# Optimization experiments

Measured on AMD Instinct MI355X. Metric: run time of the kernel, lower is better.

## Reference

```python
import jax, jax.numpy as jnp
import numpy as np

B, NP, C_IN, H = 8, 6250, 512, 256   # graphs, nodes/graph, in-feat, hidden
EPG = 100000                          # edges per graph
K = 5000                              # ceil(0.8 * NP) kept by TopKPooling
H3 = 3 * H


def setup_inputs() -> dict:
    key = jax.random.key(0)
    ks = jax.random.split(key, 16)
    N, E = B * NP, B * EPG
    x = jax.random.normal(ks[0], (N, C_IN), jnp.float32)
    offs = (jnp.arange(E) // EPG) * NP  # keep edges inside their graph
    src = jax.random.randint(ks[1], (E,), 0, NP) + offs
    dst = jax.random.randint(ks[2], (E,), 0, NP) + offs
    edge_index = jnp.stack([src, dst]).astype(jnp.int64)
    edge_attr = jax.random.uniform(ks[3], (E,), jnp.float32)
    batch = jnp.repeat(jnp.arange(B), NP).astype(jnp.int64)
    s = 0.05
    W1 = jax.random.normal(ks[4], (C_IN, H), jnp.float32) * s
    b1 = jnp.zeros((H,), jnp.float32)
    W2 = jax.random.normal(ks[5], (H, H), jnp.float32) * s
    b2 = jnp.zeros((H,), jnp.float32)
    pw = jax.random.normal(ks[6], (H3,), jnp.float32) * s   # TopKPooling attn vector
    lw1 = jax.random.normal(ks[7], (H3 * 2, H), jnp.float32) * s
    lb1 = jnp.zeros((H,), jnp.float32)
    lw2 = jax.random.normal(ks[8], (H, H // 2), jnp.float32) * s
    lb2 = jnp.zeros((H // 2,), jnp.float32)
    lw3 = jax.random.normal(ks[9], (H // 2, 3), jnp.float32) * s
    lb3 = jnp.zeros((3,), jnp.float32)
    return {"x": x, "edge_index": edge_index, "edge_attr": edge_attr, "batch": batch,
            "W1": W1, "b1": b1, "W2": W2, "b2": b2, "pw": pw,
            "lw1": lw1, "lb1": lb1, "lw2": lw2, "lb2": lb2, "lw3": lw3, "lb3": lb3}


def _gcn(x, W, b, src, dst, ew, n):
    xw = x @ W
    deg = jnp.zeros((n,), xw.dtype).at[dst].add(ew) + 1.0
    dinv = jax.lax.rsqrt(deg)
    norm = dinv[src] * ew * dinv[dst]
    out = jnp.zeros_like(xw).at[dst].add(norm[:, None] * xw[src])
    return out + (dinv * dinv)[:, None] * xw + b


def reference(x, edge_index, edge_attr, batch, W1, b1, W2, b2, pw,
              lw1, lb1, lw2, lb2, lw3, lb3):
    N = x.shape[0]
    src, dst = edge_index[0], edge_index[1]
    x1 = jax.nn.relu(_gcn(x, W1, b1, src, dst, edge_attr, N))
    x2 = jax.nn.relu(_gcn(x1, W2, b2, src, dst, edge_attr, N))
    x3 = jax.nn.relu(_gcn(x2, W2, b2, src, dst, edge_attr, N))  # conv2 reused (as in source)
    cat_x = jnp.concatenate([x1, x2, x3], axis=1)               # [N, 3H]
    # TopKPooling: score = sigmoid((x . w) / ||w||), keep top-K per graph, scale by score
    score = jax.nn.sigmoid((cat_x @ pw) / jnp.linalg.norm(pw))   # [N]
    sc = score.reshape(B, NP)
    topv, topi = jax.lax.top_k(sc, K)                            # [B, K]
    xg = cat_x.reshape(B, NP, H3)
    sel = jnp.take_along_axis(xg, topi[:, :, None], axis=1) * topv[:, :, None]  # [B, K, 3H]
    readout = jnp.concatenate([sel.mean(axis=1), sel.max(axis=1)], axis=1)      # [B, 6H]
    h = jax.nn.relu(readout @ lw1 + lb1)
    h = jax.nn.relu(h @ lw2 + lb2)       # dropout p=0 is a no-op
    return h @ lw3 + lb3                 # [B, 3]
```

## Files before the change

### kernel.cpp

```cpp
#include <hip/hip_runtime.h>
#include <stdint.h>

#define NODES  50000
#define MPAD   50048
#define NGRAPH 8
#define NP_G   6250
#define EPG    100000
#define EDGES  800000
#define KKEEP  5000
#define HID    256
#define CIN    512
#define H3     768
#define SCANB  196
#define RCHUNK 200
#define MLPCH  24
#define MLPCK  64
#define ESL    3125

#define K1_HIST  512
#define K1_CAST  25000
#define K1_W1    512
#define K1_W2    256
#define K1_TOTAL (K1_HIST + K1_CAST + K1_W1 + K1_W2 + 1)
#define GEMM_GRID 784
#define K2_GEMM  GEMM_GRID
#define K2_FILL  256
#define K2_TOTAL (K2_GEMM + K2_FILL)

using f32x4  = __attribute__((ext_vector_type(4))) float;
using bf16x8 = __attribute__((ext_vector_type(8))) short;
using u16x8  = __attribute__((ext_vector_type(8))) unsigned short;
typedef unsigned short u16;
typedef unsigned int   u32;
typedef unsigned long long u64;

__device__ __forceinline__ float bf2f(u16 u) {
    return __uint_as_float(((uint32_t)u) << 16);
}
__device__ __forceinline__ u16 f2bf(float f) {
    uint32_t u = __float_as_uint(f);
    u += 0x7fffu + ((u >> 16) & 1u);
    return (u16)(u >> 16);
}

__global__ __launch_bounds__(256) void k1_kernel(
        const int* __restrict__ ei, const float* __restrict__ ew,
        u64* __restrict__ partial,
        const float* __restrict__ x, u16* __restrict__ A0,
        const float* __restrict__ W1, const float* __restrict__ W2,
        const float* __restrict__ pw,
        u16* __restrict__ Wt1, u16* __restrict__ Wt2, float* __restrict__ invn) {
    __shared__ __align__(16) char smem[ESL * 8];
    int b = blockIdx.x, t = threadIdx.x;
    if (b < K1_HIST) {
        u64* hl = (u64*)smem;
        int g  = b >> 6;
        int r  = b & 63;
        int bb = r >> 1;
        int h  = r & 1;
        for (int k = t; k < ESL; k += 256) hl[k] = 0ull;
        __syncthreads();
        int ebase = g * EPG + bb * ESL;
        int lo = h * ESL;
        for (int k = t; k < ESL; k += 256) {
            int e = ebase + k;
            int d = ei[EDGES + e];
            int il = d - g * NP_G - lo;
            if ((unsigned)il < (unsigned)ESL) {
                u64 enc = (1ull << 48) | (u64)(ew[e] * 4294967296.0f);
                atomicAdd(&hl[il], enc);
            }
        }
        __syncthreads();
        u64* prow = partial + (size_t)(g * 32 + bb) * NP_G + lo;
        for (int k = t; k < ESL; k += 256) prow[k] = hl[k];
    } else if (b < K1_HIST + K1_CAST) {
        size_t base = ((size_t)(b - K1_HIST) * 256 + t) * 4;
        float4 v = *(const float4*)(x + base);
        ushort4 o;
        o.x = f2bf(v.x); o.y = f2bf(v.y); o.z = f2bf(v.z); o.w = f2bf(v.w);
        *(ushort4*)(A0 + base) = o;
    } else if (b < K1_HIST + K1_CAST + K1_W1) {
        int id = (b - K1_HIST - K1_CAST) * 256 + t;
        int n = id >> 9, k = id & 511;
        Wt1[id] = f2bf(W1[(size_t)k * HID + n]);
    } else if (b < K1_TOTAL - 1) {
        int id = (b - K1_HIST - K1_CAST - K1_W1) * 256 + t;
        int n = id >> 8, k = id & 255;
        Wt2[id] = f2bf(W2[(size_t)k * HID + n]);
    } else {
        float* sh = (float*)smem;
        float s = 0.f;
        for (int i = t; i < H3; i += 256) { float v = pw[i]; s += v * v; }
        sh[t] = s; __syncthreads();
        for (int off = 128; off; off >>= 1) {
            if (t < off) sh[t] += sh[t + off];
            __syncthreads();
        }
        if (t == 0) invn[0] = rsqrtf(sh[0]);
    }
}

__global__ void scan1_kernel(const u64* __restrict__ partial,
                             u32* __restrict__ blockbase,
                             int* __restrict__ iscan, int* __restrict__ bsum,
                             float* __restrict__ dinv) {
    int b = blockIdx.x, t = threadIdx.x;
    int i = b * 256 + t;
    int c = 0;
    if (i < NODES) {
        int g = i / NP_G, il = i - g * NP_G;
        size_t base = (size_t)(g * 32) * NP_G + il;
        u64 fix = 0ull; u32 cnt = 0;
#pragma unroll 4
        for (int j = 0; j < 32; ++j) {
            size_t idx = base + (size_t)j * NP_G;
            u64 pv = partial[idx];
            blockbase[idx] = cnt;
            cnt += (u32)(pv >> 48);
            fix += pv & 0xFFFFFFFFFFFFull;
        }
        c = (int)cnt;
        float deg = (float)fix * (1.0f / 4294967296.0f);
        dinv[i] = rsqrtf(deg + 1.0f);
    }
    int lane = t & 63, wv = t >> 6;
    int v = c;
    for (int off = 1; off < 64; off <<= 1) {
        int u = __shfl_up(v, off);
        if (lane >= off) v += u;
    }
    __shared__ int ws[4];
    if (lane == 63) ws[wv] = v;
    __syncthreads();
    if (t == 0) { int s = 0; for (int k = 0; k < 4; k++) { int tmp = ws[k]; ws[k] = s; s += tmp; } }
    __syncthreads();
    v += ws[wv];
    if (i < NODES) iscan[i] = v - c;
    if (t == 255) bsum[b] = v;
}

__global__ void scan2_kernel(const int* __restrict__ bsum, int* __restrict__ boff) {
    int t = threadIdx.x;
    int c = (t < SCANB) ? bsum[t] : 0;
    int lane = t & 63, wv = t >> 6;
    int v = c;
    for (int off = 1; off < 64; off <<= 1) {
        int u = __shfl_up(v, off);
        if (lane >= off) v += u;
    }
    __shared__ int ws[4];
    if (lane == 63) ws[wv] = v;
    __syncthreads();
    if (t == 0) { int s = 0; for (int k = 0; k < 4; k++) { int tmp = ws[k]; ws[k] = s; s += tmp; } }
    __syncthreads();
    v += ws[wv];
    if (t < SCANB) boff[t] = v - c;
}

__global__ void scan3_kernel(const int* __restrict__ iscan, const int* __restrict__ boff,
                             int* __restrict__ rowptr) {
    int b = blockIdx.x, t = threadIdx.x;
    int i = b * 256 + t;
    if (i > NODES) return;
    if (i == NODES) { rowptr[NODES] = EDGES; return; }
    rowptr[i] = boff[b] + iscan[i];
}

__device__ __forceinline__ bool gemm_map(int i, int& bm, int& bn) {
    int g = i & 7, s = i >> 3;
    int cnt = (g == 5) ? 48 : 49;
    if ((s >> 1) >= cnt) return false;
    bm = 49 * g - (g > 5 ? 1 : 0) + (s >> 1);
    bn = s & 1;
    return true;
}

__device__ __forceinline__ void gemm_body(const u16* __restrict__ A,
                                          const u16* __restrict__ Bt,
                                          u16* __restrict__ C,
                                          int K, int bm, int bn,
                                          u16* As, u16* Bs) {
    const int tid  = threadIdx.x;
    const int wave = tid >> 6, lane = tid & 63;
    const int wm = wave >> 1, wn = wave & 1;
    const int quad = lane >> 4, l16 = lane & 15;
    const int sr = tid >> 2;
    const int sc = tid & 3;
    const int swz = (sc ^ ((sr >> 1) & 3)) * 8;
    const int rphys = (quad ^ ((l16 >> 1) & 3)) * 8;

    const u16* Ag = A + (size_t)(bm * 128 + sr) * K + sc * 8;
    const u16* Bg = Bt + (size_t)(bn * 128 + sr) * K + sc * 8;

    f32x4 acc[4][4];
#pragma unroll
    for (int i = 0; i < 4; i++)
#pragma unroll
        for (int j = 0; j < 4; j++) { f32x4 z = {0.f, 0.f, 0.f, 0.f}; acc[i][j] = z; }

    for (int k0 = 0; k0 < K; k0 += 32) {
        int4 av0 = *(const int4*)(Ag + k0);
        int4 av1 = *(const int4*)(Ag + (size_t)64 * K + k0);
        int4 bv0 = *(const int4*)(Bg + k0);
        int4 bv1 = *(const int4*)(Bg + (size_t)64 * K + k0);
        __syncthreads();
        *(int4*)(As + sr * 32 + swz)        = av0;
        *(int4*)(As + (sr + 64) * 32 + swz) = av1;
        *(int4*)(Bs + sr * 32 + swz)        = bv0;
        *(int4*)(Bs + (sr + 64) * 32 + swz) = bv1;
        __syncthreads();
        bf16x8 af[4], bfr[4];
#pragma unroll
        for (int i = 0; i < 4; i++)
            af[i] = *(const bf16x8*)(As + (wm * 64 + i * 16 + l16) * 32 + rphys);
#pragma unroll
        for (int j = 0; j < 4; j++)
            bfr[j] = *(const bf16x8*)(Bs + (wn * 64 + j * 16 + l16) * 32 + rphys);
#pragma unroll
        for (int i = 0; i < 4; i++)
#pragma unroll
            for (int j = 0; j < 4; j++)
                acc[i][j] = __builtin_amdgcn_mfma_f32_16x16x32_bf16(af[i], bfr[j], acc[i][j], 0, 0, 0);
    }

    const int crow0 = bm * 128 + wm * 64 + quad * 4;
    const int ccol0 = bn * 128 + wn * 64 + l16;
#pragma unroll
    for (int i = 0; i < 4; i++)
#pragma unroll
        for (int j = 0; j < 4; j++)
#pragma unroll
            for (int r = 0; r < 4; r++)
                C[(size_t)(crow0 + i * 16 + r) * HID + ccol0 + j * 16] = f2bf(acc[i][j][r]);
}

__global__ __launch_bounds__(256) void k2_kernel(
        const u16* __restrict__ A0, const u16* __restrict__ Wt1, u16* __restrict__ xw,
        const int* __restrict__ ei, const float* __restrict__ ew,
        const float* __restrict__ dinv, const int* __restrict__ rowptr,
        const u32* __restrict__ blockbase, int2* __restrict__ csr) {
    __shared__ __align__(16) char smem[NP_G * 4];
    int b = blockIdx.x;
    if (b < K2_GEMM) {
        int bm, bn;
        if (!gemm_map(b, bm, bn)) return;
        u16* As = (u16*)smem;
        u16* Bs = (u16*)(smem + 8192);
        gemm_body(A0, Wt1, xw, CIN, bm, bn, As, Bs);
    } else {
        u32* cursor = (u32*)smem;
        int g  = b & 7;
        int bb = (b - K2_GEMM) >> 3;
        const u32* bbase = blockbase + (size_t)(g * 32 + bb) * NP_G;
        const int* rp = rowptr + g * NP_G;
        for (int k = threadIdx.x; k < NP_G; k += 256)
            cursor[k] = (u32)rp[k] + bbase[k];
        __syncthreads();
        int ebase = g * EPG + bb * ESL;
#pragma unroll 4
        for (int k = threadIdx.x; k < ESL; k += 256) {
            int e = ebase + k;
            int s = ei[e], d = ei[EDGES + e];
            int il = d - g * NP_G;
            u32 pos = atomicAdd(&cursor[il], 1u);
            csr[pos] = make_int2(s, __float_as_int(dinv[s] * ew[e] * dinv[d]));
        }
    }
}

__global__ __launch_bounds__(256) void gemm_bt(const u16* __restrict__ A,
                                               const u16* __restrict__ Bt,
                                               u16* __restrict__ C, int K) {
    __shared__ u16 As[128 * 32];
    __shared__ u16 Bs[128 * 32];
    int bm, bn;
    if (!gemm_map(blockIdx.x, bm, bn)) return;
    gemm_body(A, Bt, C, K, bm, bn, As, Bs);
}

template<bool SCORE>
__global__ void agg_kernel(const u16* __restrict__ xw, u16* __restrict__ xo,
                           const int* __restrict__ rowptr, const int2* __restrict__ csr,
                           const float* __restrict__ dinv, const float* __restrict__ bias,
                           const u16* __restrict__ xs1, const u16* __restrict__ xs2,
                           const float* __restrict__ pw, const float* __restrict__ invn,
                           float* __restrict__ score, u64* __restrict__ keys) {
    int wave = threadIdx.x >> 6;
    int lane = threadIdx.x & 63;
    int g  = blockIdx.x & 7;
    int nl = (blockIdx.x >> 3) * 4 + wave;
    if (nl >= NP_G) return;
    int w = g * NP_G + nl;
    int half = lane >> 5;
    int f8 = (lane & 31) * 8;
    size_t ro = (size_t)w * HID + f8;

    float acc0[8], acc1[8];
#pragma unroll
    for (int j = 0; j < 8; ++j) { acc0[j] = 0.f; acc1[j] = 0.f; }

    int p = rowptr[w], p1 = rowptr[w + 1];
    for (int q = p; q < p1; q += 64) {
        int m = min(64, p1 - q);
        int2 e = make_int2(0, 0);
        if (lane < m) e = csr[q + lane];
        int j = 0;
        for (; j + 8 <= m; j += 8) {
            int i0 = j + half,     i1 = j + 2 + half;
            int i2 = j + 4 + half, i3 = j + 6 + half;
            int   s0 = __shfl(e.x, i0, 64); float w0 = __int_as_float(__shfl(e.y, i0, 64));
            int   s1 = __shfl(e.x, i1, 64); float w1 = __int_as_float(__shfl(e.y, i1, 64));
            int   s2 = __shfl(e.x, i2, 64); float w2 = __int_as_float(__shfl(e.y, i2, 64));
            int   s3 = __shfl(e.x, i3, 64); float w3 = __int_as_float(__shfl(e.y, i3, 64));
            u16x8 v0 = *(const u16x8*)(xw + (size_t)s0 * HID + f8);
            u16x8 v1 = *(const u16x8*)(xw + (size_t)s1 * HID + f8);
            u16x8 v2 = *(const u16x8*)(xw + (size_t)s2 * HID + f8);
            u16x8 v3 = *(const u16x8*)(xw + (size_t)s3 * HID + f8);
#pragma unroll
            for (int t = 0; t < 8; ++t) {
                acc0[t] += w0 * bf2f(v0[t]);
                acc1[t] += w1 * bf2f(v1[t]);
                acc0[t] += w2 * bf2f(v2[t]);
                acc1[t] += w3 * bf2f(v3[t]);
            }
        }
        for (; j + 2 <= m; j += 2) {
            int i0 = j + half;
            int s0 = __shfl(e.x, i0, 64); float w0 = __int_as_float(__shfl(e.y, i0, 64));
            u16x8 v0 = *(const u16x8*)(xw + (size_t)s0 * HID + f8);
#pragma unroll
            for (int t = 0; t < 8; ++t) acc0[t] += w0 * bf2f(v0[t]);
        }
        if (j < m) {
            int s0 = __shfl(e.x, j, 64); float w0 = __int_as_float(__shfl(e.y, j, 64));
            w0 = half ? 0.f : w0;
            u16x8 v0 = *(const u16x8*)(xw + (size_t)s0 * HID + f8);
#pragma unroll
            for (int t = 0; t < 8; ++t) acc0[t] += w0 * bf2f(v0[t]);
        }
    }

#pragma unroll
    for (int j = 0; j < 8; ++j) {
        acc0[j] += acc1[j];
        acc0[j] += __shfl(acc0[j], lane ^ 32, 64);
    }

    float di = dinv[w], sw = di * di;
    u16x8 sv = *(const u16x8*)(xw + ro);
    float bb[8];
    {
        float4 t0 = *(const float4*)(bias + f8);
        float4 t1 = *(const float4*)(bias + f8 + 4);
        bb[0] = t0.x; bb[1] = t0.y; bb[2] = t0.z; bb[3] = t0.w;
        bb[4] = t1.x; bb[5] = t1.y; bb[6] = t1.z; bb[7] = t1.w;
    }
    u16x8 o;
    float ov[8];
#pragma unroll
    for (int j = 0; j < 8; ++j) {
        float v = fmaxf(acc0[j] + sw * bf2f(sv[j]) + bb[j], 0.f);
        o[j] = f2bf(v);
        ov[j] = bf2f(o[j]);
    }
    if (half == 0) *(u16x8*)(xo + ro) = o;

    if (SCORE) {
        u16x8 v1 = *(const u16x8*)(xs1 + ro);
        u16x8 v2 = *(const u16x8*)(xs2 + ro);
        float acc = 0.f;
#pragma unroll
        for (int j = 0; j < 8; ++j) {
            acc += bf2f(v1[j]) * pw[f8 + j];
            acc += bf2f(v2[j]) * pw[256 + f8 + j];
            acc += ov[j]       * pw[512 + f8 + j];
        }
#pragma unroll
        for (int off = 1; off < 32; off <<= 1) acc += __shfl_xor(acc, off, 64);
        if (lane == 0) {
            float s = acc * invn[0];
            float sc = 1.f / (1.f + __expf(-s));
            score[w] = sc;
            keys[w] = ((u64)__float_as_uint(sc) << 13) | (unsigned int)(NP_G - 1 - nl);
        }
    }
}

__global__ __launch_bounds__(1024) void selcomp_kernel(
        const u64* __restrict__ keys, const float* __restrict__ score,
        int* __restrict__ selidx, float* __restrict__ selscr) {
    __shared__ u64 kk[NP_G];
    __shared__ unsigned int hist[4][256];
    __shared__ unsigned int sfx[257];
    __shared__ u64 spref;
    __shared__ unsigned int swant;
    int g = blockIdx.x, t = threadIdx.x;
    const u64* kg = keys + (size_t)g * NP_G;
    for (int i = t; i < NP_G; i += 1024) kk[i] = kg[i];
    if (t == 0) { spref = 0ull; swant = KKEEP; }
    const int wgrp = (t >> 8) & 3;
    u64 mask = 0ull;
    __syncthreads();
    for (int shift = 40; shift >= 0; shift -= 8) {
        if (t < 256) { hist[0][t] = 0; hist[1][t] = 0; hist[2][t] = 0; hist[3][t] = 0; }
        __syncthreads();
        u64 pref = spref;
        for (int i = t; i < NP_G; i += 1024) {
            u64 key = kk[i];
            if ((key & mask) == pref)
                atomicAdd(&hist[wgrp][(unsigned int)(key >> shift) & 255u], 1u);
        }
        __syncthreads();
        if (t < 256) sfx[t] = hist[0][t] + hist[1][t] + hist[2][t] + hist[3][t];
        if (t == 0) sfx[256] = 0;
        __syncthreads();
        for (int off = 1; off < 256; off <<= 1) {
            unsigned int v = 0;
            if (t < 256 && t + off < 256) v = sfx[t + off];
            __syncthreads();
            if (t < 256 && t + off < 256) sfx[t] += v;
            __syncthreads();
        }
        unsigned int want = swant;
        __syncthreads();
        if (t < 256) {
            unsigned int s0 = sfx[t], s1 = sfx[t + 1];
            if (s0 >= want && s1 < want) {
                spref = pref | ((u64)t << shift);
                swant = want - s1;
            }
        }
        __syncthreads();
        mask |= (255ull << shift);
    }
    u64 kth = spref;
    int lane = t & 63, wv = t >> 6;
    __shared__ int wsum[16];
    __shared__ int cbase;
    if (t == 0) cbase = 0;
    __syncthreads();
    for (int k = 0; k < (NP_G + 1023) / 1024; ++k) {
        int i = k * 1024 + t;
        bool sel = (i < NP_G) && (kk[i] >= kth);
        int n = g * NP_G + i;
        u64 bal = __ballot(sel);
        int prefix = __popcll(bal & ((1ull << lane) - 1ull));
        if (lane == 0) wsum[wv] = __popcll(bal);
        __syncthreads();
        if (t == 0) {
            int s = cbase;
            for (int j = 0; j < 16; ++j) { int tmp = wsum[j]; wsum[j] = s; s += tmp; }
            cbase = s;
        }
        __syncthreads();
        if (sel) {
            int pos = wsum[wv] + prefix;
            selidx[g * KKEEP + pos] = n;
            selscr[g * KKEEP + pos] = score[n];
        }
        __syncthreads();
    }
}

__global__ __launch_bounds__(256) void readout_kernel(
        const u16* __restrict__ x1, const u16* __restrict__ x2,
        const u16* __restrict__ x3,
        const int* __restrict__ selidx, const float* __restrict__ selscr,
        float* __restrict__ sumbuf, int* __restrict__ maxbuf) {
    int g = blockIdx.x, tpart = blockIdx.y, c = blockIdx.z;
    int fcol = threadIdx.x;
    const u16* xt = (tpart == 0) ? x1 : ((tpart == 1) ? x2 : x3);
    __shared__ int   sidx[RCHUNK];
    __shared__ float sscr[RCHUNK];
    int base = g * KKEEP + c * RCHUNK;
    if (fcol < RCHUNK) { sidx[fcol] = selidx[base + fcol]; sscr[fcol] = selscr[base + fcol]; }
    __syncthreads();
    float sum = 0.f, mx = 0.f;
#pragma unroll 1
    for (int j = 0; j < RCHUNK; j += 4) {
        int n0 = sidx[j], n1 = sidx[j + 1], n2 = sidx[j + 2], n3 = sidx[j + 3];
        float s0 = sscr[j], s1 = sscr[j + 1], s2 = sscr[j + 2], s3 = sscr[j + 3];
        float v0 = bf2f(xt[(size_t)n0 * HID + fcol]) * s0;
        float v1 = bf2f(xt[(size_t)n1 * HID + fcol]) * s1;
        float v2 = bf2f(xt[(size_t)n2 * HID + fcol]) * s2;
        float v3 = bf2f(xt[(size_t)n3 * HID + fcol]) * s3;
        sum += v0 + v1 + v2 + v3;
        mx = fmaxf(mx, fmaxf(fmaxf(v0, v1), fmaxf(v2, v3)));
    }
    int o = (g * 3 + tpart) * HID + fcol;
    atomicAdd(&sumbuf[o], sum);
    atomicMax(&maxbuf[o], __float_as_int(mx));
}

__global__ __launch_bounds__(256) void mlp1_kernel(const float* __restrict__ sumbuf,
                                                   const int* __restrict__ maxbuf,
                                                   const float* __restrict__ lw1,
                                                   float* __restrict__ h1acc) {
    int g = blockIdx.x, ch = blockIdx.y, t = threadIdx.x;
    __shared__ float r[MLPCK];
    int k0 = ch * MLPCK;
    if (t < MLPCK) {
        int i = k0 + t;
        r[t] = (i < 768) ? sumbuf[g * 768 + i] * (1.f / 5000.f)
                         : __int_as_float(maxbuf[g * 768 + (i - 768)]);
    }
    __syncthreads();
    float a0 = 0.f, a1 = 0.f, a2 = 0.f, a3 = 0.f;
#pragma unroll
    for (int i = 0; i < MLPCK; i += 4) {
        a0 += r[i]     * lw1[(size_t)(k0 + i)     * 256 + t];
        a1 += r[i + 1] * lw1[(size_t)(k0 + i + 1) * 256 + t];
        a2 += r[i + 2] * lw1[(size_t)(k0 + i + 2) * 256 + t];
        a3 += r[i + 3] * lw1[(size_t)(k0 + i + 3) * 256 + t];
    }
    atomicAdd(&h1acc[g * 256 + t], (a0 + a1) + (a2 + a3));
}

__global__ __launch_bounds__(256) void mlp2_kernel(const float* __restrict__ h1acc,
                                                   const float* __restrict__ lb1,
                                                   const float* __restrict__ lw2,
                                                   const float* __restrict__ lb2,
                                                   const float* __restrict__ lw3,
                                                   const float* __restrict__ lb3,
                                                   float* __restrict__ out) {
    __shared__ float h1[256];
    __shared__ float part[256];
    __shared__ float h2[128];
    int g = blockIdx.x, t = threadIdx.x;
    h1[t] = fmaxf(h1acc[g * 256 + t] + lb1[t], 0.f);
    __syncthreads();
    int col = t & 127, half = t >> 7;
    float a = 0.f;
#pragma unroll
    for (int i = 0; i < 128; i += 4) {
        int k = half * 128 + i;
        a += h1[k]     * lw2[k * 128 + col]
           + h1[k + 1] * lw2[(k + 1) * 128 + col]
           + h1[k + 2] * lw2[(k + 2) * 128 + col]
           + h1[k + 3] * lw2[(k + 3) * 128 + col];
    }
    part[t] = a;
    __syncthreads();
    if (t < 128) h2[t] = fmaxf(part[t] + part[t + 128] + lb2[t], 0.f);
    __syncthreads();
    if (t < 3) {
        float a3 = lb3[t];
        for (int i = 0; i < 128; ++i) a3 += h2[i] * lw3[i * 3 + t];
        out[g * 3 + t] = a3;
    }
}

extern "C" void kernel_launch(void* const* d_in, const int* in_sizes, int n_in,
                              void* d_out, int out_size, void* d_ws, size_t ws_size,
                              hipStream_t stream) {
    const float* x   = (const float*)d_in[0];
    const int*   ei  = (const int*)d_in[1];
    const float* ew  = (const float*)d_in[2];
    const float* W1  = (const float*)d_in[4];
    const float* b1  = (const float*)d_in[5];
    const float* W2  = (const float*)d_in[6];
    const float* b2  = (const float*)d_in[7];
    const float* pw  = (const float*)d_in[8];
    const float* lw1 = (const float*)d_in[9];
    const float* lb1 = (const float*)d_in[10];
    const float* lw2 = (const float*)d_in[11];
    const float* lb2 = (const float*)d_in[12];
    const float* lw3 = (const float*)d_in[13];
    const float* lb3 = (const float*)d_in[14];
    float* out = (float*)d_out;

    char* p = (char*)d_ws;
    auto alloc = [&](size_t bytes) -> char* {
        char* r = p;
        p += (bytes + 255) & ~(size_t)255;
        return r;
    };
    u16* A0  = (u16*)alloc((size_t)MPAD * CIN * 2);
    u16* x3  = (u16*)alloc((size_t)MPAD * HID * 2);
    u16* xw  = (u16*)alloc((size_t)MPAD * HID * 2);
    u16* Wt1 = (u16*)alloc((size_t)HID * CIN * 2);
    u16* Wt2 = (u16*)alloc((size_t)HID * HID * 2);
    int2*  csr    = (int2*)alloc((size_t)EDGES * 8);
    u64*   partial   = (u64*)alloc((size_t)256 * NP_G * 8);
    u32*   blockbase = (u32*)alloc((size_t)256 * NP_G * 4);
    int*   rowptr = (int*)alloc((size_t)(NODES + 1) * 4);
    int*   iscan  = (int*)alloc((size_t)NODES * 4);
    int*   bsum   = (int*)alloc((size_t)SCANB * 4);
    int*   boff   = (int*)alloc((size_t)SCANB * 4);
    u64*   keys   = (u64*)alloc((size_t)NODES * 8);
    float* score  = (float*)alloc((size_t)NODES * 4);
    float* dinv   = (float*)alloc((size_t)NODES * 4);
    int*   selidx = (int*)alloc((size_t)NGRAPH * KKEEP * 4);
    float* selscr = (float*)alloc((size_t)NGRAPH * KKEEP * 4);
    float* invn   = (float*)alloc(256);
    char* zbase = p;
    float* sumbuf = (float*)alloc(6144 * 4);
    int*   maxbuf = (int*)alloc(6144 * 4);
    float* h1acc  = (float*)alloc((size_t)NGRAPH * 256 * 4);
    size_t zbytes = (size_t)(p - zbase);

    u16* x1 = A0;
    u16* x2 = A0 + (size_t)MPAD * HID;

    hipMemsetAsync(zbase, 0, zbytes, stream);

    k1_kernel<<<K1_TOTAL, 256, 0, stream>>>(ei, ew, partial, x, A0,
                                            W1, W2, pw, Wt1, Wt2, invn);
    scan1_kernel<<<SCANB, 256, 0, stream>>>(partial, blockbase, iscan, bsum, dinv);
    scan2_kernel<<<1, 256, 0, stream>>>(bsum, boff);
    scan3_kernel<<<SCANB + 1, 256, 0, stream>>>(iscan, boff, rowptr);
    k2_kernel<<<K2_TOTAL, 256, 0, stream>>>(A0, Wt1, xw, ei, ew, dinv, rowptr,
                                            blockbase, csr);

    int aggBlocks = 8 * ((NP_G + 3) / 4);

    agg_kernel<false><<<aggBlocks, 256, 0, stream>>>(xw, x1, rowptr, csr, dinv, b1,
                                                     nullptr, nullptr, nullptr, nullptr,
                                                     nullptr, nullptr);
    gemm_bt<<<GEMM_GRID, 256, 0, stream>>>(x1, Wt2, xw, HID);
    agg_kernel<false><<<aggBlocks, 256, 0, stream>>>(xw, x2, rowptr, csr, dinv, b2,
                                                     nullptr, nullptr, nullptr, nullptr,
                                                     nullptr, nullptr);
    gemm_bt<<<GEMM_GRID, 256, 0, stream>>>(x2, Wt2, xw, HID);
    agg_kernel<true><<<aggBlocks, 256, 0, stream>>>(xw, x3, rowptr, csr, dinv, b2,
                                                    x1, x2, pw, invn, score, keys);

    selcomp_kernel<<<NGRAPH, 1024, 0, stream>>>(keys, score, selidx, selscr);
    readout_kernel<<<dim3(NGRAPH, 3, KKEEP / RCHUNK), 256, 0, stream>>>(
        x1, x2, x3, selidx, selscr, sumbuf, maxbuf);
    mlp1_kernel<<<dim3(NGRAPH, MLPCH), 256, 0, stream>>>(sumbuf, maxbuf, lw1, h1acc);
    mlp2_kernel<<<NGRAPH, 256, 0, stream>>>(h1acc, lb1, lw2, lb2, lw3, lb3, out);
}
```

Measured before the change: 462.8 us.

## Fuse fp32-to-bf16 cast into first GEMM, merge scan passes, unroll aggregation

Drops the separate pass that cast the node-feature matrix to bf16 and wrote it out. The first GEMM now loads fp32 rows and converts them in registers with packed bf16 conversion instructions, which removes one full write and re-read of a large intermediate. The scan2 kernel is folded into scan3: each block sums the preceding block totals itself, saving one launch at the cost of redundant reductions. The aggregation loop gains a 16-edge unrolled path to put more gathers in flight, which raises register pressure. The GEMM now also reads twice as many A bytes per tile.

```diff
diff --git a/kernel.cpp b/kernel.cpp
--- a/kernel.cpp
+++ b/kernel.cpp
@@ -18,10 +18,9 @@
 #define ESL    3125
 
 #define K1_HIST  512
-#define K1_CAST  25000
 #define K1_W1    512
 #define K1_W2    256
-#define K1_TOTAL (K1_HIST + K1_CAST + K1_W1 + K1_W2 + 1)
+#define K1_TOTAL (K1_HIST + K1_W1 + K1_W2 + 1)
 #define GEMM_GRID 784
 #define K2_GEMM  GEMM_GRID
 #define K2_FILL  256
@@ -42,11 +41,18 @@
     u += 0x7fffu + ((u >> 16) & 1u);
     return (u16)(u >> 16);
 }
+__device__ __forceinline__ int4 f32x8_to_bf16x8(float4 a, float4 b) {
+    int4 r;
+    asm("v_cvt_pk_bf16_f32 %0, %1, %2" : "=v"(r.x) : "v"(a.x), "v"(a.y));
+    asm("v_cvt_pk_bf16_f32 %0, %1, %2" : "=v"(r.y) : "v"(a.z), "v"(a.w));
+    asm("v_cvt_pk_bf16_f32 %0, %1, %2" : "=v"(r.z) : "v"(b.x), "v"(b.y));
+    asm("v_cvt_pk_bf16_f32 %0, %1, %2" : "=v"(r.w) : "v"(b.z), "v"(b.w));
+    return r;
+}
 
 __global__ __launch_bounds__(256) void k1_kernel(
         const int* __restrict__ ei, const float* __restrict__ ew,
         u64* __restrict__ partial,
-        const float* __restrict__ x, u16* __restrict__ A0,
         const float* __restrict__ W1, const float* __restrict__ W2,
         const float* __restrict__ pw,
         u16* __restrict__ Wt1, u16* __restrict__ Wt2, float* __restrict__ invn) {
@@ -74,18 +80,12 @@
         __syncthreads();
         u64* prow = partial + (size_t)(g * 32 + bb) * NP_G + lo;
         for (int k = t; k < ESL; k += 256) prow[k] = hl[k];
-    } else if (b < K1_HIST + K1_CAST) {
-        size_t base = ((size_t)(b - K1_HIST) * 256 + t) * 4;
-        float4 v = *(const float4*)(x + base);
-        ushort4 o;
-        o.x = f2bf(v.x); o.y = f2bf(v.y); o.z = f2bf(v.z); o.w = f2bf(v.w);
-        *(ushort4*)(A0 + base) = o;
-    } else if (b < K1_HIST + K1_CAST + K1_W1) {
-        int id = (b - K1_HIST - K1_CAST) * 256 + t;
+    } else if (b < K1_HIST + K1_W1) {
+        int id = (b - K1_HIST) * 256 + t;
         int n = id >> 9, k = id & 511;
         Wt1[id] = f2bf(W1[(size_t)k * HID + n]);
     } else if (b < K1_TOTAL - 1) {
-        int id = (b - K1_HIST - K1_CAST - K1_W1) * 256 + t;
+        int id = (b - K1_HIST - K1_W1) * 256 + t;
         int n = id >> 8, k = id & 255;
         Wt2[id] = f2bf(W2[(size_t)k * HID + n]);
     } else {
@@ -140,31 +140,19 @@
     if (t == 255) bsum[b] = v;
 }
 
-__global__ void scan2_kernel(const int* __restrict__ bsum, int* __restrict__ boff) {
-    int t = threadIdx.x;
-    int c = (t < SCANB) ? bsum[t] : 0;
-    int lane = t & 63, wv = t >> 6;
-    int v = c;
-    for (int off = 1; off < 64; off <<= 1) {
-        int u = __shfl_up(v, off);
-        if (lane >= off) v += u;
-    }
-    __shared__ int ws[4];
-    if (lane == 63) ws[wv] = v;
-    __syncthreads();
-    if (t == 0) { int s = 0; for (int k = 0; k < 4; k++) { int tmp = ws[k]; ws[k] = s; s += tmp; } }
-    __syncthreads();
-    v += ws[wv];
-    if (t < SCANB) boff[t] = v - c;
-}
-
-__global__ void scan3_kernel(const int* __restrict__ iscan, const int* __restrict__ boff,
+__global__ void scan3_kernel(const int* __restrict__ iscan, const int* __restrict__ bsum,
                              int* __restrict__ rowptr) {
     int b = blockIdx.x, t = threadIdx.x;
+    int v = (t < b) ? bsum[t] : 0;
+    for (int off = 1; off < 64; off <<= 1) v += __shfl_xor(v, off, 64);
+    __shared__ int ws[4];
+    if ((t & 63) == 0) ws[t >> 6] = v;
+    __syncthreads();
+    int boffb = ws[0] + ws[1] + ws[2] + ws[3];
     int i = b * 256 + t;
     if (i > NODES) return;
     if (i == NODES) { rowptr[NODES] = EDGES; return; }
-    rowptr[i] = boff[b] + iscan[i];
+    rowptr[i] = boffb + iscan[i];
 }
 
 __device__ __forceinline__ bool gemm_map(int i, int& bm, int& bn) {
@@ -235,8 +223,74 @@
                 C[(size_t)(crow0 + i * 16 + r) * HID + ccol0 + j * 16] = f2bf(acc[i][j][r]);
 }
 
+__device__ __forceinline__ void gemm_body_f32A(const float* __restrict__ X,
+                                               const u16* __restrict__ Bt,
+                                               u16* __restrict__ C,
+                                               int bm, int bn,
+                                               u16* As, u16* Bs) {
+    const int tid  = threadIdx.x;
+    const int wave = tid >> 6, lane = tid & 63;
+    const int wm = wave >> 1, wn = wave & 1;
+    const int quad = lane >> 4, l16 = lane & 15;
+    const int sr = tid >> 2;
+    const int sc = tid & 3;
+    const int swz = (sc ^ ((sr >> 1) & 3)) * 8;
+    const int rphys = (quad ^ ((l16 >> 1) & 3)) * 8;
+
+    int r0 = bm * 128 + sr;      if (r0 > NODES - 1) r0 = NODES - 1;
+    int r1 = bm * 128 + sr + 64; if (r1 > NODES - 1) r1 = NODES - 1;
+    const float* Ag0 = X + (size_t)r0 * CIN + sc * 8;
+    const float* Ag1 = X + (size_t)r1 * CIN + sc * 8;
+    const u16*   Bg  = Bt + (size_t)(bn * 128 + sr) * CIN + sc * 8;
+
+    f32x4 acc[4][4];
+#pragma unroll
+    for (int i = 0; i < 4; i++)
+#pragma unroll
+        for (int j = 0; j < 4; j++) { f32x4 z = {0.f, 0.f, 0.f, 0.f}; acc[i][j] = z; }
+
+    for (int k0 = 0; k0 < CIN; k0 += 32) {
+        float4 a00 = *(const float4*)(Ag0 + k0);
+        float4 a01 = *(const float4*)(Ag0 + k0 + 4);
+        float4 a10 = *(const float4*)(Ag1 + k0);
+        float4 a11 = *(const float4*)(Ag1 + k0 + 4);
+        int4 bv0 = *(const int4*)(Bg + k0);
+        int4 bv1 = *(const int4*)(Bg + (size_t)64 * CIN + k0);
+        int4 av0 = f32x8_to_bf16x8(a00, a01);
+        int4 av1 = f32x8_to_bf16x8(a10, a11);
+        __syncthreads();
+        *(int4*)(As + sr * 32 + swz)        = av0;
+        *(int4*)(As + (sr + 64) * 32 + swz) = av1;
+        *(int4*)(Bs + sr * 32 + swz)        = bv0;
+        *(int4*)(Bs + (sr + 64) * 32 + swz) = bv1;
+        __syncthreads();
+        bf16x8 af[4], bfr[4];
+#pragma unroll
+        for (int i = 0; i < 4; i++)
+            af[i] = *(const bf16x8*)(As + (wm * 64 + i * 16 + l16) * 32 + rphys);
+#pragma unroll
+        for (int j = 0; j < 4; j++)
+            bfr[j] = *(const bf16x8*)(Bs + (wn * 64 + j * 16 + l16) * 32 + rphys);
+#pragma unroll
+        for (int i = 0; i < 4; i++)
+#pragma unroll
+            for (int j = 0; j < 4; j++)
+                acc[i][j] = __builtin_amdgcn_mfma_f32_16x16x32_bf16(af[i], bfr[j], acc[i][j], 0, 0, 0);
+    }
+
+    const int crow0 = bm * 128 + wm * 64 + quad * 4;
+    const int ccol0 = bn * 128 + wn * 64 + l16;
+#pragma unroll
+    for (int i = 0; i < 4; i++)
+#pragma unroll
+        for (int j = 0; j < 4; j++)
+#pragma unroll
+            for (int r = 0; r < 4; r++)
+                C[(size_t)(crow0 + i * 16 + r) * HID + ccol0 + j * 16] = f2bf(acc[i][j][r]);
+}
+
 __global__ __launch_bounds__(256) void k2_kernel(
-        const u16* __restrict__ A0, const u16* __restrict__ Wt1, u16* __restrict__ xw,
+        const float* __restrict__ x, const u16* __restrict__ Wt1, u16* __restrict__ xw,
         const int* __restrict__ ei, const float* __restrict__ ew,
         const float* __restrict__ dinv, const int* __restrict__ rowptr,
         const u32* __restrict__ blockbase, int2* __restrict__ csr) {
@@ -247,7 +301,7 @@
         if (!gemm_map(b, bm, bn)) return;
         u16* As = (u16*)smem;
         u16* Bs = (u16*)(smem + 8192);
-        gemm_body(A0, Wt1, xw, CIN, bm, bn, As, Bs);
+        gemm_body_f32A(x, Wt1, xw, bm, bn, As, Bs);
     } else {
         u32* cursor = (u32*)smem;
         int g  = b & 7;
@@ -306,6 +360,27 @@
         int2 e = make_int2(0, 0);
         if (lane < m) e = csr[q + lane];
         int j = 0;
+        for (; j + 16 <= m; j += 16) {
+            int   s[8]; float wt[8];
+#pragma unroll
+            for (int k = 0; k < 8; ++k) {
+                int idx = j + 2 * k + half;
+                s[k]  = __shfl(e.x, idx, 64);
+                wt[k] = __int_as_float(__shfl(e.y, idx, 64));
+            }
+            u16x8 v[8];
+#pragma unroll
+            for (int k = 0; k < 8; ++k)
+                v[k] = *(const u16x8*)(xw + (size_t)s[k] * HID + f8);
+#pragma unroll
+            for (int k = 0; k < 8; k += 2) {
+#pragma unroll
+                for (int t = 0; t < 8; ++t) {
+                    acc0[t] += wt[k]     * bf2f(v[k][t]);
+                    acc1[t] += wt[k + 1] * bf2f(v[k + 1][t]);
+                }
+            }
+        }
         for (; j + 8 <= m; j += 8) {
             int i0 = j + half,     i1 = j + 2 + half;
             int i2 = j + 4 + half, i3 = j + 6 + half;
@@ -587,7 +662,6 @@
     int*   rowptr = (int*)alloc((size_t)(NODES + 1) * 4);
     int*   iscan  = (int*)alloc((size_t)NODES * 4);
     int*   bsum   = (int*)alloc((size_t)SCANB * 4);
-    int*   boff   = (int*)alloc((size_t)SCANB * 4);
     u64*   keys   = (u64*)alloc((size_t)NODES * 8);
     float* score  = (float*)alloc((size_t)NODES * 4);
     float* dinv   = (float*)alloc((size_t)NODES * 4);
@@ -605,12 +679,11 @@
 
     hipMemsetAsync(zbase, 0, zbytes, stream);
 
-    k1_kernel<<<K1_TOTAL, 256, 0, stream>>>(ei, ew, partial, x, A0,
+    k1_kernel<<<K1_TOTAL, 256, 0, stream>>>(ei, ew, partial,
                                             W1, W2, pw, Wt1, Wt2, invn);
     scan1_kernel<<<SCANB, 256, 0, stream>>>(partial, blockbase, iscan, bsum, dinv);
-    scan2_kernel<<<1, 256, 0, stream>>>(bsum, boff);
-    scan3_kernel<<<SCANB + 1, 256, 0, stream>>>(iscan, boff, rowptr);
-    k2_kernel<<<K2_TOTAL, 256, 0, stream>>>(A0, Wt1, xw, ei, ew, dinv, rowptr,
+    scan3_kernel<<<SCANB + 1, 256, 0, stream>>>(iscan, bsum, rowptr);
+    k2_kernel<<<K2_TOTAL, 256, 0, stream>>>(x, Wt1, xw, ei, ew, dinv, rowptr,
                                             blockbase, csr);
 
     int aggBlocks = 8 * ((NP_G + 3) / 4);
```

Result: slower. 472.7 us (+2.1%).

## Split GEMM and CSR fill kernels, shrink GEMM tile, fold scan2 into scan3

Applied to the files above, without the earlier changes.

Shrinks the bf16 MFMA GEMM tile from 128x128 to 64x128 rows per block, doubling the grid and cutting LDS and accumulator registers so more blocks fit per CU. The first GEMM no longer shares a launch with the CSR fill. The fill becomes its own kernel that uses a half-size shared cursor array and makes two passes over each edge slice. The separate scan2 launch is dropped: each scan3 block reduces the preceding block sums itself. This saves a launch at the cost of redundant reductions, and the fill now reads the destination indices twice.

```diff
diff --git a/kernel.cpp b/kernel.cpp
--- a/kernel.cpp
+++ b/kernel.cpp
@@ -22,10 +22,8 @@
 #define K1_W1    512
 #define K1_W2    256
 #define K1_TOTAL (K1_HIST + K1_CAST + K1_W1 + K1_W2 + 1)
-#define GEMM_GRID 784
-#define K2_GEMM  GEMM_GRID
-#define K2_FILL  256
-#define K2_TOTAL (K2_GEMM + K2_FILL)
+#define GEMM_GRID 1568
+#define FILL_GRID 256
 
 using f32x4  = __attribute__((ext_vector_type(4))) float;
 using bf16x8 = __attribute__((ext_vector_type(8))) short;
@@ -140,143 +138,136 @@
     if (t == 255) bsum[b] = v;
 }
 
-__global__ void scan2_kernel(const int* __restrict__ bsum, int* __restrict__ boff) {
-    int t = threadIdx.x;
-    int c = (t < SCANB) ? bsum[t] : 0;
-    int lane = t & 63, wv = t >> 6;
-    int v = c;
-    for (int off = 1; off < 64; off <<= 1) {
-        int u = __shfl_up(v, off);
-        if (lane >= off) v += u;
-    }
-    __shared__ int ws[4];
-    if (lane == 63) ws[wv] = v;
-    __syncthreads();
-    if (t == 0) { int s = 0; for (int k = 0; k < 4; k++) { int tmp = ws[k]; ws[k] = s; s += tmp; } }
-    __syncthreads();
-    v += ws[wv];
-    if (t < SCANB) boff[t] = v - c;
-}
-
-__global__ void scan3_kernel(const int* __restrict__ iscan, const int* __restrict__ boff,
+__global__ void scan3_kernel(const int* __restrict__ iscan, const int* __restrict__ bsum,
                              int* __restrict__ rowptr) {
     int b = blockIdx.x, t = threadIdx.x;
+    int v = (t < b) ? bsum[t] : 0;
+    for (int off = 1; off < 64; off <<= 1) v += __shfl_xor(v, off, 64);
+    __shared__ int ws[4];
+    if ((t & 63) == 0) ws[t >> 6] = v;
+    __syncthreads();
+    int boffb = ws[0] + ws[1] + ws[2] + ws[3];
     int i = b * 256 + t;
     if (i > NODES) return;
     if (i == NODES) { rowptr[NODES] = EDGES; return; }
-    rowptr[i] = boff[b] + iscan[i];
-}
-
-__device__ __forceinline__ bool gemm_map(int i, int& bm, int& bn) {
+    rowptr[i] = boffb + iscan[i];
+}
+
+__device__ __forceinline__ bool gemm_map64(int i, int& bm, int& bn) {
     int g = i & 7, s = i >> 3;
-    int cnt = (g == 5) ? 48 : 49;
-    if ((s >> 1) >= cnt) return false;
-    bm = 49 * g - (g > 5 ? 1 : 0) + (s >> 1);
+    int b0 = (6250 * g + 63) >> 6;
+    int b1 = (6250 * (g + 1) + 63) >> 6;
+    int t = b0 + (s >> 1);
+    if (t >= b1) return false;
+    bm = t;
     bn = s & 1;
     return true;
 }
 
-__device__ __forceinline__ void gemm_body(const u16* __restrict__ A,
-                                          const u16* __restrict__ Bt,
-                                          u16* __restrict__ C,
-                                          int K, int bm, int bn,
-                                          u16* As, u16* Bs) {
+__device__ __forceinline__ void gemm64_body(const u16* __restrict__ A,
+                                            const u16* __restrict__ Bt,
+                                            u16* __restrict__ C,
+                                            int K, int bm, int bn,
+                                            u16* As, u16* Bs) {
     const int tid  = threadIdx.x;
     const int wave = tid >> 6, lane = tid & 63;
-    const int wm = wave >> 1, wn = wave & 1;
     const int quad = lane >> 4, l16 = lane & 15;
     const int sr = tid >> 2;
     const int sc = tid & 3;
     const int swz = (sc ^ ((sr >> 1) & 3)) * 8;
     const int rphys = (quad ^ ((l16 >> 1) & 3)) * 8;
 
-    const u16* Ag = A + (size_t)(bm * 128 + sr) * K + sc * 8;
+    const u16* Ag = A + (size_t)(bm * 64 + sr) * K + sc * 8;
     const u16* Bg = Bt + (size_t)(bn * 128 + sr) * K + sc * 8;
 
-    f32x4 acc[4][4];
+    f32x4 acc[4][2];
 #pragma unroll
     for (int i = 0; i < 4; i++)
 #pragma unroll
-        for (int j = 0; j < 4; j++) { f32x4 z = {0.f, 0.f, 0.f, 0.f}; acc[i][j] = z; }
+        for (int j = 0; j < 2; j++) { f32x4 z = {0.f, 0.f, 0.f, 0.f}; acc[i][j] = z; }
 
     for (int k0 = 0; k0 < K; k0 += 32) {
         int4 av0 = *(const int4*)(Ag + k0);
-        int4 av1 = *(const int4*)(Ag + (size_t)64 * K + k0);
         int4 bv0 = *(const int4*)(Bg + k0);
         int4 bv1 = *(const int4*)(Bg + (size_t)64 * K + k0);
         __syncthreads();
         *(int4*)(As + sr * 32 + swz)        = av0;
-        *(int4*)(As + (sr + 64) * 32 + swz) = av1;
         *(int4*)(Bs + sr * 32 + swz)        = bv0;
         *(int4*)(Bs + (sr + 64) * 32 + swz) = bv1;
         __syncthreads();
-        bf16x8 af[4], bfr[4];
+        bf16x8 af[4], bfr[2];
 #pragma unroll
         for (int i = 0; i < 4; i++)
-            af[i] = *(const bf16x8*)(As + (wm * 64 + i * 16 + l16) * 32 + rphys);
-#pragma unroll
-        for (int j = 0; j < 4; j++)
-            bfr[j] = *(const bf16x8*)(Bs + (wn * 64 + j * 16 + l16) * 32 + rphys);
+            af[i] = *(const bf16x8*)(As + (i * 16 + l16) * 32 + rphys);
+#pragma unroll
+        for (int j = 0; j < 2; j++)
+            bfr[j] = *(const bf16x8*)(Bs + (wave * 32 + j * 16 + l16) * 32 + rphys);
 #pragma unroll
         for (int i = 0; i < 4; i++)
 #pragma unroll
-            for (int j = 0; j < 4; j++)
+            for (int j = 0; j < 2; j++)
                 acc[i][j] = __builtin_amdgcn_mfma_f32_16x16x32_bf16(af[i], bfr[j], acc[i][j], 0, 0, 0);
     }
 
-    const int crow0 = bm * 128 + wm * 64 + quad * 4;
-    const int ccol0 = bn * 128 + wn * 64 + l16;
+    const int crow0 = bm * 64 + quad * 4;
+    const int ccol0 = bn * 128 + wave * 32 + l16;
 #pragma unroll
     for (int i = 0; i < 4; i++)
 #pragma unroll
-        for (int j = 0; j < 4; j++)
+        for (int j = 0; j < 2; j++)
 #pragma unroll
             for (int r = 0; r < 4; r++)
                 C[(size_t)(crow0 + i * 16 + r) * HID + ccol0 + j * 16] = f2bf(acc[i][j][r]);
 }
 
 __global__ __launch_bounds__(256) void k2_kernel(
-        const u16* __restrict__ A0, const u16* __restrict__ Wt1, u16* __restrict__ xw,
+        const u16* __restrict__ A0, const u16* __restrict__ Wt1,
+        u16* __restrict__ C) {
+    __shared__ u16 As[64 * 32];
+    __shared__ u16 Bs[128 * 32];
+    int bm, bn;
+    if (!gemm_map64(blockIdx.x, bm, bn)) return;
+    gemm64_body(A0, Wt1, C, CIN, bm, bn, As, Bs);
+}
+
+__global__ __launch_bounds__(256) void gemm_bt(const u16* __restrict__ A,
+                                               const u16* __restrict__ Bt,
+                                               u16* __restrict__ C, int K) {
+    __shared__ u16 As[64 * 32];
+    __shared__ u16 Bs[128 * 32];
+    int bm, bn;
+    if (!gemm_map64(blockIdx.x, bm, bn)) return;
+    gemm64_body(A, Bt, C, K, bm, bn, As, Bs);
+}
+
+__global__ __launch_bounds__(256) void fill_kernel(
         const int* __restrict__ ei, const float* __restrict__ ew,
         const float* __restrict__ dinv, const int* __restrict__ rowptr,
         const u32* __restrict__ blockbase, int2* __restrict__ csr) {
-    __shared__ __align__(16) char smem[NP_G * 4];
-    int b = blockIdx.x;
-    if (b < K2_GEMM) {
-        int bm, bn;
-        if (!gemm_map(b, bm, bn)) return;
-        u16* As = (u16*)smem;
-        u16* Bs = (u16*)(smem + 8192);
-        gemm_body(A0, Wt1, xw, CIN, bm, bn, As, Bs);
-    } else {
-        u32* cursor = (u32*)smem;
-        int g  = b & 7;
-        int bb = (b - K2_GEMM) >> 3;
-        const u32* bbase = blockbase + (size_t)(g * 32 + bb) * NP_G;
-        const int* rp = rowptr + g * NP_G;
-        for (int k = threadIdx.x; k < NP_G; k += 256)
-            cursor[k] = (u32)rp[k] + bbase[k];
-        __syncthreads();
-        int ebase = g * EPG + bb * ESL;
+    __shared__ u32 cursor[ESL];
+    int g  = blockIdx.x & 7;
+    int bb = blockIdx.x >> 3;
+    const u32* bbase = blockbase + (size_t)(g * 32 + bb) * NP_G;
+    const int* rp = rowptr + g * NP_G;
+    int ebase = g * EPG + bb * ESL;
+    for (int h = 0; h < 2; ++h) {
+        int lo = h * ESL;
+        for (int k = threadIdx.x; k < ESL; k += 256)
+            cursor[k] = (u32)rp[lo + k] + bbase[lo + k];
+        __syncthreads();
 #pragma unroll 4
         for (int k = threadIdx.x; k < ESL; k += 256) {
             int e = ebase + k;
-            int s = ei[e], d = ei[EDGES + e];
-            int il = d - g * NP_G;
-            u32 pos = atomicAdd(&cursor[il], 1u);
-            csr[pos] = make_int2(s, __float_as_int(dinv[s] * ew[e] * dinv[d]));
-        }
-    }
-}
-
-__global__ __launch_bounds__(256) void gemm_bt(const u16* __restrict__ A,
-                                               const u16* __restrict__ Bt,
-                                               u16* __restrict__ C, int K) {
-    __shared__ u16 As[128 * 32];
-    __shared__ u16 Bs[128 * 32];
-    int bm, bn;
-    if (!gemm_map(blockIdx.x, bm, bn)) return;
-    gemm_body(A, Bt, C, K, bm, bn, As, Bs);
+            int d = ei[EDGES + e];
+            int il = d - g * NP_G - lo;
+            if ((unsigned)il < (unsigned)ESL) {
+                int s = ei[e];
+                u32 pos = atomicAdd(&cursor[il], 1u);
+                csr[pos] = make_int2(s, __float_as_int(dinv[s] * ew[e] * dinv[d]));
+            }
+        }
+        __syncthreads();
+    }
 }
 
 template<bool SCORE>
@@ -587,7 +578,6 @@
     int*   rowptr = (int*)alloc((size_t)(NODES + 1) * 4);
     int*   iscan  = (int*)alloc((size_t)NODES * 4);
     int*   bsum   = (int*)alloc((size_t)SCANB * 4);
-    int*   boff   = (int*)alloc((size_t)SCANB * 4);
     u64*   keys   = (u64*)alloc((size_t)NODES * 8);
     float* score  = (float*)alloc((size_t)NODES * 4);
     float* dinv   = (float*)alloc((size_t)NODES * 4);
@@ -608,10 +598,9 @@
     k1_kernel<<<K1_TOTAL, 256, 0, stream>>>(ei, ew, partial, x, A0,
                                             W1, W2, pw, Wt1, Wt2, invn);
     scan1_kernel<<<SCANB, 256, 0, stream>>>(partial, blockbase, iscan, bsum, dinv);
-    scan2_kernel<<<1, 256, 0, stream>>>(bsum, boff);
-    scan3_kernel<<<SCANB + 1, 256, 0, stream>>>(iscan, boff, rowptr);
-    k2_kernel<<<K2_TOTAL, 256, 0, stream>>>(A0, Wt1, xw, ei, ew, dinv, rowptr,
-                                            blockbase, csr);
+    scan3_kernel<<<SCANB + 1, 256, 0, stream>>>(iscan, bsum, rowptr);
+    k2_kernel<<<GEMM_GRID, 256, 0, stream>>>(A0, Wt1, xw);
+    fill_kernel<<<FILL_GRID, 256, 0, stream>>>(ei, ew, dinv, rowptr, blockbase, csr);
 
     int aggBlocks = 8 * ((NP_G + 3) / 4);
 
```

Result: no change. 469.0 us (+1.3%).
